# Kernel tuning notes

Hardware: AMD Instinct MI355X
Metric: run time of the kernel (lower is better)

The kernel has to match this reference:

```python
import jax, jax.numpy as jnp
import numpy as np

N_SAMPLES = 8_000_000
N_TRAIN = 1_000_000
KS = 9
HALF_KS = (KS - 1) // 2  # 4
SIGMA = 1.0


def _build_stats():
    """Replicates LDSLoss.__init__: histogramdd, gaussian LDS smoothing, scaling."""
    rng = np.random.default_rng(0)
    labels = rng.uniform(0.0, 10.0, size=(N_TRAIN, 2))
    n_bins = int((labels.max() - labels.min()) / 0.1)
    hist, edges = np.histogramdd(labels, bins=n_bins)
    # gaussian_filter1d(impulse, sigma)/max == exp(-0.5*(x/sigma)^2), truncated at 4*sigma (= half_ks)
    x = np.arange(-HALF_KS, HALF_KS + 1, dtype=np.float64)
    kernel = np.exp(-0.5 * (x / SIGMA) ** 2)
    # scipy.ndimage.convolve1d(hist, kernel, mode='constant') acts along the LAST axis only;
    # kernel is symmetric so convolution == correlation.
    pad = np.pad(hist, ((0, 0), (HALF_KS, HALF_KS)))
    smoothed = np.zeros_like(hist)
    for k in range(KS):
        smoothed += kernel[k] * pad[:, k:k + n_bins]
    bins0 = edges[0]
    bins1 = edges[1]
    # scaling = len(w)/sum(w) with w = 1/smoothed[bin(label)] over the training labels
    i0 = np.clip(np.searchsorted(bins0, labels[:, 0], side='right') - 1, 0, n_bins - 1)
    i1 = np.clip(np.searchsorted(bins1, labels[:, 1], side='right') - 1, 0, n_bins - 1)
    w = 1.0 / smoothed[i0, i1]
    scaling = len(w) / w.sum()
    lo = np.array([bins0[0], bins1[0]])
    hi = np.array([bins0[-1], bins1[-1]])
    return (smoothed.astype(np.float32), bins0.astype(np.float32),
            bins1.astype(np.float32), np.float32(scaling), lo, hi)


def setup_inputs() -> dict:
    smoothed, bins0, bins1, scaling, lo, hi = _build_stats()
    key = jax.random.key(0)
    k1, k2 = jax.random.split(key)
    inp = jax.random.normal(k1, (N_SAMPLES, 2), dtype=jnp.float32)
    # targets drawn inside the training-label range (as histogram bins cover it)
    tgt = jax.random.uniform(k2, (N_SAMPLES, 2), dtype=jnp.float32,
                             minval=jnp.asarray(lo, jnp.float32),
                             maxval=jnp.asarray(hi, jnp.float32))
    return {
        "input": inp,
        "target": tgt,
        "smoothed_distribution": jnp.asarray(smoothed),
        "bins0": jnp.asarray(bins0),
        "bins1": jnp.asarray(bins1),
        "scaling": jnp.asarray(scaling),
    }


def reference(input, target, smoothed_distribution, bins0, bins1, scaling):
    nb = smoothed_distribution.shape[0]
    # torch.where(label < bins)[0][0] - 1  ==  searchsorted(bins, label, 'right') - 1,
    # with the 'no edge greater' case mapped to the last bin (len(bins)-2).
    i0 = jnp.clip(jnp.searchsorted(bins0, target[:, 0], side='right') - 1, 0, nb - 1)
    i1 = jnp.clip(jnp.searchsorted(bins1, target[:, 1], side='right') - 1, 0, nb - 1)
    kernel_weights = smoothed_distribution[i0, i1]          # irregular gather  [N]
    weights = 1.0 / kernel_weights
    inf_mask = jnp.isinf(weights)
    finite_max = jnp.max(jnp.where(inf_mask, -jnp.inf, weights))
    weights = jnp.where(inf_mask, finite_max, weights) * scaling
    loss = (input - target) ** 2                             # MSELoss(reduction='none')
    loss = loss * weights[:, None]
    return jnp.mean(loss)
```

## Files before the change

### kernel.cpp

```cpp
#include <hip/hip_runtime.h>
#include <math.h>


#define BLOCK 512
#define GRID_BLKS 1024

__device__ __forceinline__ int find_bin(const float2* __restrict__ ep, int nb,
                                        float x, float lo, float inv_step) {
    int g = (int)floorf((x - lo) * inv_step);
    g = g < 0 ? 0 : (g > nb - 1 ? nb - 1 : g);
    float2 e = ep[g];
    g += (x >= e.y) ? 1 : 0;
    g -= (x < e.x) ? 1 : 0;
    return g < 0 ? 0 : (g > nb - 1 ? nb - 1 : g);
}

__device__ __forceinline__ void process_pair(
    float4 in, float4 tg,
    float* __restrict__ hist,
    const float2* __restrict__ ep0, const float2* __restrict__ ep1, int nb,
    float lo0, float inv0, float lo1, float inv1)
{
    float dA0 = in.x - tg.x, dA1 = in.y - tg.y;
    float sqA = dA0 * dA0 + dA1 * dA1;
    int iA0 = find_bin(ep0, nb, tg.x, lo0, inv0);
    int iA1 = find_bin(ep1, nb, tg.y, lo1, inv1);
    atomicAdd(&hist[iA0 * nb + iA1], sqA);

    float dB0 = in.z - tg.z, dB1 = in.w - tg.w;
    float sqB = dB0 * dB0 + dB1 * dB1;
    int iB0 = find_bin(ep0, nb, tg.z, lo0, inv0);
    int iB1 = find_bin(ep1, nb, tg.w, lo1, inv1);
    atomicAdd(&hist[iB0 * nb + iB1], sqB);
}

__global__ void __launch_bounds__(BLOCK, 4)
lds_loss_hist(const float* __restrict__ input,
              const float* __restrict__ target,
              const float* __restrict__ smoothed,
              const float* __restrict__ bins0,
              const float* __restrict__ bins1,
              const float* __restrict__ scaling,
              int nb, long long n, long long nelem,
              double* __restrict__ accA,
              double* __restrict__ accB,
              unsigned int* __restrict__ accM,
              unsigned int* __restrict__ done_ctr,
              float* __restrict__ out)
{
    extern __shared__ __align__(16) float smem[];
    float2* ep0  = (float2*)smem;
    float2* ep1  = ep0 + nb;
    float*  hist = (float*)(ep1 + nb);

    const int nbnb = nb * nb;
    for (int i = threadIdx.x; i < nbnb; i += BLOCK) hist[i] = 0.0f;
    for (int i = threadIdx.x; i < nb; i += BLOCK) {
        ep0[i] = make_float2(bins0[i], bins0[i + 1]);
        ep1[i] = make_float2(bins1[i], bins1[i + 1]);
    }
    __syncthreads();

    const float lo0 = ep0[0].x, hi0 = ep0[nb - 1].y;
    const float lo1 = ep1[0].x, hi1 = ep1[nb - 1].y;
    const float inv0 = (float)nb / (hi0 - lo0);
    const float inv1 = (float)nb / (hi1 - lo1);

    const long long npair = n >> 1;
    const float4* in4 = (const float4*)input;
    const float4* tg4 = (const float4*)target;
    const long long S = (long long)gridDim.x * BLOCK;

    long long p = (long long)blockIdx.x * BLOCK + threadIdx.x;

    for (; p + 3 * S < npair; p += 4 * S) {
        float4 I0 = in4[p];
        float4 I1 = in4[p + S];
        float4 I2 = in4[p + 2 * S];
        float4 I3 = in4[p + 3 * S];
        float4 T0 = tg4[p];
        float4 T1 = tg4[p + S];
        float4 T2 = tg4[p + 2 * S];
        float4 T3 = tg4[p + 3 * S];
        __builtin_amdgcn_sched_barrier(0);
        process_pair(I0, T0, hist, ep0, ep1, nb, lo0, inv0, lo1, inv1);
        process_pair(I1, T1, hist, ep0, ep1, nb, lo0, inv0, lo1, inv1);
        process_pair(I2, T2, hist, ep0, ep1, nb, lo0, inv0, lo1, inv1);
        process_pair(I3, T3, hist, ep0, ep1, nb, lo0, inv0, lo1, inv1);
    }
    for (; p < npair; p += S) {
        process_pair(in4[p], tg4[p], hist, ep0, ep1, nb, lo0, inv0, lo1, inv1);
    }

    if ((n & 1) && blockIdx.x == 0 && threadIdx.x == 0) {
        long long i = n - 1;
        float t0 = target[2 * i], t1 = target[2 * i + 1];
        float d0 = input[2 * i] - t0, d1 = input[2 * i + 1] - t1;
        float sq = d0 * d0 + d1 * d1;
        int j0 = find_bin(ep0, nb, t0, lo0, inv0);
        int j1 = find_bin(ep1, nb, t1, lo1, inv1);
        atomicAdd(&hist[j0 * nb + j1], sq);
    }
    __syncthreads();

    double A = 0.0, B = 0.0;
    float  m = 0.0f;
    for (int b = threadIdx.x; b < nbnb; b += BLOCK) {
        float h = hist[b];
        float s = smoothed[b];
        float w = 1.0f / s;
        if (isinf(w)) {
            B += (double)h;
        } else {
            A += (double)w * (double)h;
            if (h > 0.0f) m = fmaxf(m, w);
        }
    }

    #pragma unroll
    for (int off = 32; off > 0; off >>= 1) {
        A += __shfl_down(A, off, 64);
        B += __shfl_down(B, off, 64);
        m = fmaxf(m, __shfl_down(m, off, 64));
    }

    __shared__ double rA[BLOCK / 64], rB[BLOCK / 64];
    __shared__ float  rM[BLOCK / 64];
    int wave = threadIdx.x >> 6;
    int lane = threadIdx.x & 63;
    if (lane == 0) { rA[wave] = A; rB[wave] = B; rM[wave] = m; }
    __syncthreads();

    if (threadIdx.x == 0) {
        double ta = 0.0, tb = 0.0; float tm = 0.0f;
        #pragma unroll
        for (int w2 = 0; w2 < BLOCK / 64; ++w2) {
            ta += rA[w2]; tb += rB[w2]; tm = fmaxf(tm, rM[w2]);
        }
        atomicAdd(accA, ta);
        atomicAdd(accB, tb);
        atomicMax(accM, __float_as_uint(tm));
        __threadfence();
        unsigned int prev = atomicAdd(done_ctr, 1u);
        if (prev == gridDim.x - 1) {
            double Af = atomicAdd(accA, 0.0);
            double Bf = atomicAdd(accB, 0.0);
            float  Mf = __uint_as_float(atomicMax(accM, 0u));
            double v = (double)(*scaling) * (Af + (double)Mf * Bf) / (double)nelem;
            *out = (float)v;
        }
    }
}

extern "C" void kernel_launch(void* const* d_in, const int* in_sizes, int n_in,
                              void* d_out, int out_size, void* d_ws, size_t ws_size,
                              hipStream_t stream) {
    const float* input    = (const float*)d_in[0];
    const float* target   = (const float*)d_in[1];
    const float* smoothed = (const float*)d_in[2];
    const float* bins0    = (const float*)d_in[3];
    const float* bins1    = (const float*)d_in[4];
    const float* scaling  = (const float*)d_in[5];

    const long long nelem = in_sizes[0];
    const long long n     = nelem / 2;
    const int nb          = in_sizes[3] - 1;

    double*       accA = (double*)d_ws;
    double*       accB = accA + 1;
    unsigned int* accM = (unsigned int*)(accB + 1);
    unsigned int* ctr  = accM + 1;

    hipMemsetAsync(d_ws, 0, 24, stream);

    long long blocks_needed = (n / 2 + BLOCK - 1) / BLOCK;
    int grid = (int)(blocks_needed < GRID_BLKS ? blocks_needed : GRID_BLKS);
    if (grid < 1) grid = 1;
    size_t shmem = ((size_t)nb * nb + 4 * (size_t)nb) * sizeof(float);

    lds_loss_hist<<<grid, BLOCK, shmem, stream>>>(
        input, target, smoothed, bins0, bins1, scaling,
        nb, n, nelem, accA, accB, accM, ctr, (float*)d_out);
}
```

Measured before the change: 207.3 us.

## Software-pipeline streaming loads with inline asm and explicit vmcnt waits

```diff
diff --git a/kernel.cpp b/kernel.cpp
--- a/kernel.cpp
+++ b/kernel.cpp
@@ -3,7 +3,18 @@
 
 
 #define BLOCK 512
-#define GRID_BLKS 1024
+#define GRID_BLKS 768
+#define NSLOT 12
+
+typedef __attribute__((ext_vector_type(4))) float f32x4;
+
+#define GLOAD(dst, ptr) \
+    asm volatile("global_load_dwordx4 %0, %1, off" : "=v"(dst) : "v"(ptr))
+#define WAITVM(N)                                             \
+    {                                                         \
+        asm volatile("s_waitcnt vmcnt(" #N ")" ::: "memory"); \
+        __builtin_amdgcn_sched_barrier(0);                    \
+    }
 
 __device__ __forceinline__ int find_bin(const float2* __restrict__ ep, int nb,
                                         float x, float lo, float inv_step) {
@@ -16,25 +27,28 @@
 }
 
 __device__ __forceinline__ void process_pair(
-    float4 in, float4 tg,
+    f32x4 in, f32x4 tg, bool valid,
     float* __restrict__ hist,
     const float2* __restrict__ ep0, const float2* __restrict__ ep1, int nb,
     float lo0, float inv0, float lo1, float inv1)
 {
-    float dA0 = in.x - tg.x, dA1 = in.y - tg.y;
+    float dA0 = in[0] - tg[0], dA1 = in[1] - tg[1];
     float sqA = dA0 * dA0 + dA1 * dA1;
-    int iA0 = find_bin(ep0, nb, tg.x, lo0, inv0);
-    int iA1 = find_bin(ep1, nb, tg.y, lo1, inv1);
-    atomicAdd(&hist[iA0 * nb + iA1], sqA);
-
-    float dB0 = in.z - tg.z, dB1 = in.w - tg.w;
+    int iA0 = find_bin(ep0, nb, tg[0], lo0, inv0);
+    int iA1 = find_bin(ep1, nb, tg[1], lo1, inv1);
+
+    float dB0 = in[2] - tg[2], dB1 = in[3] - tg[3];
     float sqB = dB0 * dB0 + dB1 * dB1;
-    int iB0 = find_bin(ep0, nb, tg.z, lo0, inv0);
-    int iB1 = find_bin(ep1, nb, tg.w, lo1, inv1);
-    atomicAdd(&hist[iB0 * nb + iB1], sqB);
-}
-
-__global__ void __launch_bounds__(BLOCK, 4)
+    int iB0 = find_bin(ep0, nb, tg[2], lo0, inv0);
+    int iB1 = find_bin(ep1, nb, tg[3], lo1, inv1);
+
+    if (valid) {
+        atomicAdd(&hist[iA0 * nb + iA1], sqA);
+        atomicAdd(&hist[iB0 * nb + iB1], sqB);
+    }
+}
+
+__global__ void __launch_bounds__(BLOCK)
 lds_loss_hist(const float* __restrict__ input,
               const float* __restrict__ target,
               const float* __restrict__ smoothed,
@@ -67,29 +81,57 @@
     const float inv1 = (float)nb / (hi1 - lo1);
 
     const long long npair = n >> 1;
-    const float4* in4 = (const float4*)input;
-    const float4* tg4 = (const float4*)target;
+    const f32x4* in4 = (const f32x4*)input;
+    const f32x4* tg4 = (const f32x4*)target;
     const long long S = (long long)gridDim.x * BLOCK;
 
-    long long p = (long long)blockIdx.x * BLOCK + threadIdx.x;
-
-    for (; p + 3 * S < npair; p += 4 * S) {
-        float4 I0 = in4[p];
-        float4 I1 = in4[p + S];
-        float4 I2 = in4[p + 2 * S];
-        float4 I3 = in4[p + 3 * S];
-        float4 T0 = tg4[p];
-        float4 T1 = tg4[p + S];
-        float4 T2 = tg4[p + 2 * S];
-        float4 T3 = tg4[p + 3 * S];
-        __builtin_amdgcn_sched_barrier(0);
-        process_pair(I0, T0, hist, ep0, ep1, nb, lo0, inv0, lo1, inv1);
-        process_pair(I1, T1, hist, ep0, ep1, nb, lo0, inv0, lo1, inv1);
-        process_pair(I2, T2, hist, ep0, ep1, nb, lo0, inv0, lo1, inv1);
-        process_pair(I3, T3, hist, ep0, ep1, nb, lo0, inv0, lo1, inv1);
-    }
-    for (; p < npair; p += S) {
-        process_pair(in4[p], tg4[p], hist, ep0, ep1, nb, lo0, inv0, lo1, inv1);
+    const long long MACRO = (long long)NSLOT * S;
+    const long long niter = (npair + MACRO - 1) / MACRO;
+
+    long long base = (long long)blockIdx.x * BLOCK + threadIdx.x;
+
+    for (long long it = 0; it < niter; ++it, base += MACRO) {
+        const f32x4* aI[NSLOT];
+        const f32x4* aT[NSLOT];
+        bool         vv[NSLOT];
+        #pragma unroll
+        for (int j = 0; j < NSLOT; ++j) {
+            long long q = base + (long long)j * S;
+            vv[j] = q < npair;
+            q = vv[j] ? q : (npair - 1);
+            aI[j] = in4 + q;
+            aT[j] = tg4 + q;
+        }
+
+        f32x4 A0, A1, A2, A3, Ax0, Ax1, Ax2, Ax3;
+        f32x4 B0, B1, B2, B3, Bx0, Bx1, Bx2, Bx3;
+        f32x4 C0, C1, C2, C3, Cx0, Cx1, Cx2, Cx3;
+
+        GLOAD(A0, aI[0]);  GLOAD(A1, aI[1]);  GLOAD(A2, aI[2]);  GLOAD(A3, aI[3]);
+        GLOAD(Ax0, aT[0]); GLOAD(Ax1, aT[1]); GLOAD(Ax2, aT[2]); GLOAD(Ax3, aT[3]);
+        GLOAD(B0, aI[4]);  GLOAD(B1, aI[5]);  GLOAD(B2, aI[6]);  GLOAD(B3, aI[7]);
+        GLOAD(Bx0, aT[4]); GLOAD(Bx1, aT[5]); GLOAD(Bx2, aT[6]); GLOAD(Bx3, aT[7]);
+
+        WAITVM(8);
+        process_pair(A0, Ax0, vv[0], hist, ep0, ep1, nb, lo0, inv0, lo1, inv1);
+        process_pair(A1, Ax1, vv[1], hist, ep0, ep1, nb, lo0, inv0, lo1, inv1);
+        process_pair(A2, Ax2, vv[2], hist, ep0, ep1, nb, lo0, inv0, lo1, inv1);
+        process_pair(A3, Ax3, vv[3], hist, ep0, ep1, nb, lo0, inv0, lo1, inv1);
+
+        GLOAD(C0, aI[8]);  GLOAD(C1, aI[9]);  GLOAD(C2, aI[10]); GLOAD(C3, aI[11]);
+        GLOAD(Cx0, aT[8]); GLOAD(Cx1, aT[9]); GLOAD(Cx2, aT[10]); GLOAD(Cx3, aT[11]);
+
+        WAITVM(8);
+        process_pair(B0, Bx0, vv[4], hist, ep0, ep1, nb, lo0, inv0, lo1, inv1);
+        process_pair(B1, Bx1, vv[5], hist, ep0, ep1, nb, lo0, inv0, lo1, inv1);
+        process_pair(B2, Bx2, vv[6], hist, ep0, ep1, nb, lo0, inv0, lo1, inv1);
+        process_pair(B3, Bx3, vv[7], hist, ep0, ep1, nb, lo0, inv0, lo1, inv1);
+
+        WAITVM(0);
+        process_pair(C0, Cx0, vv[8],  hist, ep0, ep1, nb, lo0, inv0, lo1, inv1);
+        process_pair(C1, Cx1, vv[9],  hist, ep0, ep1, nb, lo0, inv0, lo1, inv1);
+        process_pair(C2, Cx2, vv[10], hist, ep0, ep1, nb, lo0, inv0, lo1, inv1);
+        process_pair(C3, Cx3, vv[11], hist, ep0, ep1, nb, lo0, inv0, lo1, inv1);
     }
 
     if ((n & 1) && blockIdx.x == 0 && threadIdx.x == 0) {
```

After: 197.4 us. 4.8% less time.
